# Kernel optimization log

Hardware: AMD Instinct MI355X
Metric: run time of the kernel (lower is better)

Reference implementation:

```python
import jax, jax.numpy as jnp
import numpy as np

NEIGH = 0.4  # neighborhood_size from the module


def setup_inputs() -> dict:
    key = jax.random.key(0)
    ks = jax.random.split(key, 14)
    N, E, H, G, M = 1024, 64, 128, 8, 20
    OUT = 6 * M
    f32 = jnp.float32
    inp = {
        "xabs": jax.random.uniform(ks[0], (N, 2), f32),
        "i_h0": jax.random.normal(ks[1], (1, N, H), f32) * 0.1,
        "i_c0": jax.random.normal(ks[2], (1, N, H), f32) * 0.1,
        # I_Embedding: Linear(2, E)
        "W_emb": jax.random.normal(ks[3], (E, 2), f32) * 0.5,
        "b_emb": jax.random.normal(ks[4], (E,), f32) * 0.1,
        # embedding_social: Linear(G*G*H, E)
        "W_soc": jax.random.normal(ks[5], (E, G * G * H), f32) * (1.0 / np.sqrt(G * G * H)),
        "b_soc": jax.random.normal(ks[6], (E,), f32) * 0.1,
        # LSTM(2E -> H), torch gate order [i, f, g, o]
        "W_ih": jax.random.normal(ks[7], (4 * H, 2 * E), f32) * (1.0 / np.sqrt(2 * E)),
        "W_hh": jax.random.normal(ks[8], (4 * H, H), f32) * (1.0 / np.sqrt(H)),
        "b_ih": jax.random.normal(ks[9], (4 * H,), f32) * 0.05,
        "b_hh": jax.random.normal(ks[10], (4 * H,), f32) * 0.05,
        # I_Output: Linear(H, 6*M)
        "W_out": jax.random.normal(ks[11], (OUT, H), f32) * (1.0 / np.sqrt(H)),
        "b_out": jax.random.normal(ks[12], (OUT,), f32) * 0.05,
    }
    return inp


def _grid_mask(xabs, G):
    # Vectorized getGridMask: [N, N, G*G] one-hot bin membership.
    N = xabs.shape[0]
    # dx[n, m] = other_x - width_low(n); in-range iff 0 <= dx < NEIGH
    dx = xabs[None, :, 0] - (xabs[:, None, 0] - NEIGH / 2)
    dy = xabs[None, :, 1] - (xabs[:, None, 1] - NEIGH / 2)
    cell_x = jnp.floor(dx / NEIGH * G).astype(jnp.int32)
    cell_y = jnp.floor(dy / NEIGH * G).astype(jnp.int32)
    valid = (dx >= 0) & (dx < NEIGH) & (dy >= 0) & (dy < NEIGH)
    valid &= (cell_x >= 0) & (cell_x < G) & (cell_y >= 0) & (cell_y < G)
    valid &= ~jnp.eye(N, dtype=bool)  # skip self
    cell = jnp.where(valid, cell_x + cell_y * G, 0)
    mask = jax.nn.one_hot(cell, G * G, dtype=xabs.dtype)
    return mask * valid[:, :, None].astype(xabs.dtype)


def reference(xabs, i_h0, i_c0, W_emb, b_emb, W_soc, b_soc,
              W_ih, W_hh, b_ih, b_hh, W_out, b_out):
    N = xabs.shape[0]
    H = i_h0.shape[-1]
    G = int(np.sqrt(W_soc.shape[1] // H))
    M = W_out.shape[0] // 6

    # Input embedding
    emb_x = jax.nn.relu(xabs @ W_emb.T + b_emb)  # [N, E]

    # Social pooling: grid mask + scatter-reduce of hidden states
    h0 = i_h0[0]  # [N, H]
    mask = _grid_mask(xabs, G)  # [N, N, G*G]
    social = jnp.einsum('nmg,md->ngd', mask, h0)  # [N, G*G, H]
    social = social.reshape(N, G * G * H)
    pooling = jax.nn.relu(social @ W_soc.T + b_soc)  # [N, E]

    # Single LSTM step (seq len 1, 1 layer), torch gate order i,f,g,o
    lstm_in = jnp.concatenate([emb_x, pooling], axis=-1)  # [N, 2E]
    gates = lstm_in @ W_ih.T + b_ih + h0 @ W_hh.T + b_hh  # [N, 4H]
    i_g, f_g, g_g, o_g = jnp.split(gates, 4, axis=-1)
    c = jax.nn.sigmoid(f_g) * i_c0[0] + jax.nn.sigmoid(i_g) * jnp.tanh(g_g)
    h = jax.nn.sigmoid(o_g) * jnp.tanh(c)  # [N, H]

    final = h @ W_out.T + b_out  # [N, 6M]
    mu1, mu2, log_sigma1, log_sigma2, rho, pi_logits = jnp.split(final, 6, axis=1)
    return (mu1, mu2, log_sigma1, log_sigma2, rho, pi_logits)
```

## Files before the change

kernel.cpp:

```cpp
#include <hip/hip_runtime.h>
#include <hip/hip_bf16.h>
#include <math.h>

typedef __hip_bfloat16 bf16;
typedef short s8v __attribute__((ext_vector_type(8)));
typedef float f4v __attribute__((ext_vector_type(4)));

__device__ __forceinline__ float b2f(bf16 v) { return __bfloat162float(v); }

template <bool F32>
__device__ __forceinline__ float ld(const void* p, int i) {
  if (F32) return ((const float*)p)[i];
  return b2f(((const bf16*)p)[i]);
}

template <bool F32>
__device__ __forceinline__ s8v ldfrag(const void* p, size_t i) {
  if (F32) {
    const float* f = (const float*)p + i;
    float4 u = *reinterpret_cast<const float4*>(f);
    float4 v = *reinterpret_cast<const float4*>(f + 4);
    s8v r;
    bf16 t;
    t = __float2bfloat16(u.x); r[0] = *(short*)&t;
    t = __float2bfloat16(u.y); r[1] = *(short*)&t;
    t = __float2bfloat16(u.z); r[2] = *(short*)&t;
    t = __float2bfloat16(u.w); r[3] = *(short*)&t;
    t = __float2bfloat16(v.x); r[4] = *(short*)&t;
    t = __float2bfloat16(v.y); r[5] = *(short*)&t;
    t = __float2bfloat16(v.z); r[6] = *(short*)&t;
    t = __float2bfloat16(v.w); r[7] = *(short*)&t;
    return r;
  }
  return *reinterpret_cast<const s8v*>((const bf16*)p + i);
}

__device__ __forceinline__ float sigm(float x) {
  return 0.5f * (1.0f + tanhf(0.5f * x));
}

__device__ __forceinline__ bool detect_f32(const void* xabs) {
  unsigned short v = ((const unsigned short*)xabs)[threadIdx.x & 63];
  int ex = (v >> 7) & 0xFF;
  return __ballot(ex >= 0x93) != 0ull;
}

template <bool F32>
__device__ __forceinline__ void cvt4(const void* src, bf16* __restrict__ dst,
                                     int count, int gt, int gsz) {
  for (int i = gt * 4; i < count; i += gsz * 4) {
    if (F32) {
      float4 v = *reinterpret_cast<const float4*>((const float*)src + i);
      bf16 t[4] = {__float2bfloat16(v.x), __float2bfloat16(v.y),
                   __float2bfloat16(v.z), __float2bfloat16(v.w)};
      *reinterpret_cast<uint2*>(&dst[i]) = *reinterpret_cast<uint2*>(t);
    } else {
      *reinterpret_cast<uint2*>(&dst[i]) =
          *reinterpret_cast<const uint2*>((const bf16*)src + i);
    }
  }
}

__global__ __launch_bounds__(256) void k_prep(const void* Wsoc, const void* Wih,
                                              const void* Whh, const void* Wout,
                                              bf16* Wsoc_b, bf16* Wih_b,
                                              bf16* Whh_b, bf16* Wout_b,
                                              const void* xabs) {
  const int gt = blockIdx.x * 256 + threadIdx.x;
  const int gsz = gridDim.x * 256;
  if (detect_f32(xabs)) {
    cvt4<true>(Wsoc, Wsoc_b, 64 * 8192, gt, gsz);
    cvt4<true>(Wih, Wih_b, 512 * 128, gt, gsz);
    cvt4<true>(Whh, Whh_b, 512 * 128, gt, gsz);
    cvt4<true>(Wout, Wout_b, 120 * 128, gt, gsz);
  } else {
    cvt4<false>(Wsoc, Wsoc_b, 64 * 8192, gt, gsz);
    cvt4<false>(Wih, Wih_b, 512 * 128, gt, gsz);
    cvt4<false>(Whh, Whh_b, 512 * 128, gt, gsz);
    cvt4<false>(Wout, Wout_b, 120 * 128, gt, gsz);
  }
}

template <bool F32>
__device__ __forceinline__ void zgemm_body(const void* h0,
                                           const bf16* __restrict__ Wsoc_b,
                                           bf16* __restrict__ Z) {
  const int wave = threadIdx.x >> 6, lane = threadIdx.x & 63;
  const int mt = blockIdx.x & 63;
  const int g  = (blockIdx.x >> 6) * 4 + wave;
  const int r16 = lane & 15, quad = lane >> 4;
  s8v afr[4];
#pragma unroll
  for (int kq = 0; kq < 4; ++kq)
    afr[kq] = ldfrag<F32>(h0, (size_t)(mt * 16 + r16) * 128 + kq * 32 + quad * 8);
  f4v acc[4] = {{0.f, 0.f, 0.f, 0.f}, {0.f, 0.f, 0.f, 0.f},
                {0.f, 0.f, 0.f, 0.f}, {0.f, 0.f, 0.f, 0.f}};
#pragma unroll
  for (int t = 0; t < 4; ++t) {
#pragma unroll
    for (int kq = 0; kq < 4; ++kq) {
      s8v bfr = *reinterpret_cast<const s8v*>(
          &Wsoc_b[(size_t)(t * 16 + r16) * 8192 + g * 128 + kq * 32 + quad * 8]);
      acc[t] = __builtin_amdgcn_mfma_f32_16x16x32_bf16(afr[kq], bfr, acc[t],
                                                       0, 0, 0);
    }
  }
#pragma unroll
  for (int t = 0; t < 4; ++t)
#pragma unroll
    for (int reg = 0; reg < 4; ++reg)
      Z[(size_t)(mt * 16 + quad * 4 + reg) * 4096 + g * 64 + t * 16 + r16] =
          __float2bfloat16(acc[t][reg]);
}

__global__ __launch_bounds__(256) void k_zgemm(const void* h0,
                                               const bf16* Wsoc_b,
                                               bf16* __restrict__ Z,
                                               const void* xabs) {
  if (detect_f32(xabs)) zgemm_body<true>(h0, Wsoc_b, Z);
  else                  zgemm_body<false>(h0, Wsoc_b, Z);
}

#define XS 264
#define HS 136

template <bool F32>
__device__ __forceinline__ void fused_body(
    const void* xabs, const void* h0, const void* Wemb, const void* bemb,
    const void* bsoc, const bf16* __restrict__ Wih_b,
    const bf16* __restrict__ Whh_b, const void* bih, const void* bhh,
    const void* c0, const bf16* __restrict__ Wout_b, const void* bout,
    const bf16* __restrict__ Z, void* out, char* smem) {
  float* G   = (float*)smem;
  int* lists = (int*)smem;
  bf16* Xb   = (bf16*)(smem + 32768);
  bf16* Hb   = (bf16*)(smem + 32768 + 16 * XS * 2);
  const int tid = threadIdx.x;
  const int wave = tid >> 6, lane = tid & 63;
  const int r16 = lane & 15, quad = lane >> 4;

  for (int idx = 4 * XS + tid; idx < 16 * XS; idx += 256)
    Xb[idx] = __float2bfloat16(0.f);
  for (int idx = 4 * HS + tid; idx < 16 * HS; idx += 256)
    Hb[idx] = __float2bfloat16(0.f);

  const int n = blockIdx.x * 4 + wave;
  const float xn = ld<F32>(xabs, 2 * n);
  const float yn = ld<F32>(xabs, 2 * n + 1);
  const float tx = xn - 0.2f, ty = yn - 0.2f;
  int* mylist = lists + wave * 1024;
  int cnt = 0;
  for (int c = 0; c < 16; ++c) {
    const int m = c * 64 + lane;
    float dx = ld<F32>(xabs, 2 * m) - tx;
    float dy = ld<F32>(xabs, 2 * m + 1) - ty;
    int cx = (int)floorf(dx / 0.4f * 8.0f);
    int cy = (int)floorf(dy / 0.4f * 8.0f);
    bool valid = (dx >= 0.f) & (dx < 0.4f) & (dy >= 0.f) & (dy < 0.4f) &
                 (cx >= 0) & (cx < 8) & (cy >= 0) & (cy < 8) & (m != n);
    unsigned long long msk = __ballot(valid);
    if (valid) {
      int pos = cnt + __popcll(msk & ((1ull << lane) - 1ull));
      mylist[pos] = (m << 6) | (cx + cy * 8);
    }
    cnt += __popcll(msk);
  }
  float a0 = 0.f, a1 = 0.f, a2 = 0.f, a3 = 0.f;
  float a4 = 0.f, a5 = 0.f, a6 = 0.f, a7 = 0.f;
  int i = 0;
  for (; i + 8 <= cnt; i += 8) {
    int e0 = mylist[i],     e1 = mylist[i + 1];
    int e2 = mylist[i + 2], e3 = mylist[i + 3];
    int e4 = mylist[i + 4], e5 = mylist[i + 5];
    int e6 = mylist[i + 6], e7 = mylist[i + 7];
    a0 += b2f(Z[(size_t)(e0 >> 6) * 4096 + (e0 & 63) * 64 + lane]);
    a1 += b2f(Z[(size_t)(e1 >> 6) * 4096 + (e1 & 63) * 64 + lane]);
    a2 += b2f(Z[(size_t)(e2 >> 6) * 4096 + (e2 & 63) * 64 + lane]);
    a3 += b2f(Z[(size_t)(e3 >> 6) * 4096 + (e3 & 63) * 64 + lane]);
    a4 += b2f(Z[(size_t)(e4 >> 6) * 4096 + (e4 & 63) * 64 + lane]);
    a5 += b2f(Z[(size_t)(e5 >> 6) * 4096 + (e5 & 63) * 64 + lane]);
    a6 += b2f(Z[(size_t)(e6 >> 6) * 4096 + (e6 & 63) * 64 + lane]);
    a7 += b2f(Z[(size_t)(e7 >> 6) * 4096 + (e7 & 63) * 64 + lane]);
  }
  for (; i < cnt; ++i) {
    int e0 = mylist[i];
    a0 += b2f(Z[(size_t)(e0 >> 6) * 4096 + (e0 & 63) * 64 + lane]);
  }
  float pool = ((a0 + a1) + (a2 + a3)) + ((a4 + a5) + (a6 + a7));
  pool = fmaxf(pool + ld<F32>(bsoc, lane), 0.f);
  float emb = fmaxf(ld<F32>(Wemb, lane * 2) * xn +
                        ld<F32>(Wemb, lane * 2 + 1) * yn + ld<F32>(bemb, lane),
                    0.f);
  Xb[wave * XS + lane] = __float2bfloat16(emb);
  Xb[wave * XS + 64 + lane] = __float2bfloat16(pool);
  Xb[wave * XS + 128 + lane] = __float2bfloat16(ld<F32>(h0, n * 128 + lane));
  Xb[wave * XS + 192 + lane] =
      __float2bfloat16(ld<F32>(h0, n * 128 + 64 + lane));
  __syncthreads();

  s8v afr[8];
#pragma unroll
  for (int kq = 0; kq < 8; ++kq)
    afr[kq] = *reinterpret_cast<const s8v*>(&Xb[r16 * XS + kq * 32 + quad * 8]);
  const int j0w = wave * 128;
  f4v bacc[8];
#pragma unroll
  for (int jt = 0; jt < 8; ++jt) bacc[jt] = (f4v){0.f, 0.f, 0.f, 0.f};
#pragma unroll
  for (int jt = 0; jt < 8; ++jt) {
    int j = j0w + jt * 16 + r16;
#pragma unroll
    for (int kq = 0; kq < 4; ++kq) {
      s8v bfr = *reinterpret_cast<const s8v*>(
          &Wih_b[(size_t)j * 128 + kq * 32 + quad * 8]);
      bacc[jt] = __builtin_amdgcn_mfma_f32_16x16x32_bf16(afr[kq], bfr, bacc[jt],
                                                         0, 0, 0);
    }
#pragma unroll
    for (int kq = 0; kq < 4; ++kq) {
      s8v bfr = *reinterpret_cast<const s8v*>(
          &Whh_b[(size_t)j * 128 + kq * 32 + quad * 8]);
      bacc[jt] = __builtin_amdgcn_mfma_f32_16x16x32_bf16(afr[kq + 4], bfr,
                                                         bacc[jt], 0, 0, 0);
    }
  }
#pragma unroll
  for (int jt = 0; jt < 8; ++jt) {
    int j = j0w + jt * 16 + r16;
    float bias = ld<F32>(bih, j) + ld<F32>(bhh, j);
#pragma unroll
    for (int reg = 0; reg < 4; ++reg)
      G[(quad * 4 + reg) * 512 + j] = bacc[jt][reg] + bias;
  }
  __syncthreads();

  for (int idx = tid; idx < 512; idx += 256) {
    int m = idx >> 7, tt = idx & 127;
    float ig = G[m * 512 + tt], fg = G[m * 512 + 128 + tt];
    float gg = G[m * 512 + 256 + tt], og = G[m * 512 + 384 + tt];
    float c = sigm(fg) * ld<F32>(c0, (blockIdx.x * 4 + m) * 128 + tt) +
              sigm(ig) * tanhf(gg);
    Hb[m * HS + tt] = __float2bfloat16(sigm(og) * tanhf(c));
  }
  __syncthreads();

  s8v hfr[4];
#pragma unroll
  for (int kq = 0; kq < 4; ++kq)
    hfr[kq] = *reinterpret_cast<const s8v*>(&Hb[r16 * HS + kq * 32 + quad * 8]);
#pragma unroll
  for (int jt2 = 0; jt2 < 2; ++jt2) {
    int j = wave * 32 + jt2 * 16 + r16;
    int jj = j < 120 ? j : 119;
    f4v oacc = (f4v){0.f, 0.f, 0.f, 0.f};
#pragma unroll
    for (int kq = 0; kq < 4; ++kq) {
      s8v bfr = *reinterpret_cast<const s8v*>(
          &Wout_b[(size_t)jj * 128 + kq * 32 + quad * 8]);
      oacc = __builtin_amdgcn_mfma_f32_16x16x32_bf16(hfr[kq], bfr, oacc, 0, 0, 0);
    }
    if (j < 120 && quad == 0) {
      float bo = ld<F32>(bout, j);
      int kk = j / 20, mm = j % 20;
#pragma unroll
      for (int reg = 0; reg < 4; ++reg) {
        int oi = kk * 20480 + (blockIdx.x * 4 + reg) * 20 + mm;
        float val = oacc[reg] + bo;
        if (F32) ((float*)out)[oi] = val;
        else     ((bf16*)out)[oi] = __float2bfloat16(val);
      }
    }
  }
}

__global__ __launch_bounds__(256, 1) void k_fused(
    const void* xabs, const void* h0, const void* Wemb, const void* bemb,
    const void* bsoc, const bf16* Wih_b, const bf16* Whh_b, const void* bih,
    const void* bhh, const void* c0, const bf16* Wout_b, const void* bout,
    const bf16* __restrict__ Z, void* out) {
  __shared__ __align__(16) char smem[32768 + 16 * XS * 2 + 16 * HS * 2];
  if (detect_f32(xabs))
    fused_body<true>(xabs, h0, Wemb, bemb, bsoc, Wih_b, Whh_b, bih, bhh, c0,
                     Wout_b, bout, Z, out, smem);
  else
    fused_body<false>(xabs, h0, Wemb, bemb, bsoc, Wih_b, Whh_b, bih, bhh, c0,
                      Wout_b, bout, Z, out, smem);
}

extern "C" void kernel_launch(void* const* d_in, const int* in_sizes, int n_in,
                              void* d_out, int out_size, void* d_ws, size_t ws_size,
                              hipStream_t stream) {
  const void* xabs = d_in[0];
  const void* h0   = d_in[1];
  const void* c0   = d_in[2];
  const void* Wemb = d_in[3];
  const void* bemb = d_in[4];
  const void* Wsoc = d_in[5];
  const void* bsoc = d_in[6];
  const void* Wih  = d_in[7];
  const void* Whh  = d_in[8];
  const void* bih  = d_in[9];
  const void* bhh  = d_in[10];
  const void* Wout = d_in[11];
  const void* bout = d_in[12];

  bf16* Z      = (bf16*)d_ws;
  bf16* Wsoc_b = Z + (size_t)1024 * 4096;
  bf16* Wih_b  = Wsoc_b + (size_t)64 * 8192;
  bf16* Whh_b  = Wih_b + (size_t)512 * 128;
  bf16* Wout_b = Whh_b + (size_t)512 * 128;

  k_prep<<<dim3(128), dim3(256), 0, stream>>>(Wsoc, Wih, Whh, Wout, Wsoc_b,
                                              Wih_b, Whh_b, Wout_b, xabs);
  k_zgemm<<<dim3(1024), dim3(256), 0, stream>>>(h0, Wsoc_b, Z, xabs);
  k_fused<<<dim3(256), dim3(256), 0, stream>>>(xabs, h0, Wemb, bemb, bsoc,
                                               Wih_b, Whh_b, bih, bhh, c0,
                                               Wout_b, bout, Z, d_out);
}
```

Before: 129.3 us.

## Fold weight conversion into Z-GEMM and raise per-block M tiling

```diff
diff --git a/kernel.cpp b/kernel.cpp
--- a/kernel.cpp
+++ b/kernel.cpp
@@ -61,64 +61,69 @@
   }
 }
 
-__global__ __launch_bounds__(256) void k_prep(const void* Wsoc, const void* Wih,
-                                              const void* Whh, const void* Wout,
-                                              bf16* Wsoc_b, bf16* Wih_b,
-                                              bf16* Whh_b, bf16* Wout_b,
-                                              const void* xabs) {
-  const int gt = blockIdx.x * 256 + threadIdx.x;
-  const int gsz = gridDim.x * 256;
-  if (detect_f32(xabs)) {
-    cvt4<true>(Wsoc, Wsoc_b, 64 * 8192, gt, gsz);
-    cvt4<true>(Wih, Wih_b, 512 * 128, gt, gsz);
-    cvt4<true>(Whh, Whh_b, 512 * 128, gt, gsz);
-    cvt4<true>(Wout, Wout_b, 120 * 128, gt, gsz);
-  } else {
-    cvt4<false>(Wsoc, Wsoc_b, 64 * 8192, gt, gsz);
-    cvt4<false>(Wih, Wih_b, 512 * 128, gt, gsz);
-    cvt4<false>(Whh, Whh_b, 512 * 128, gt, gsz);
-    cvt4<false>(Wout, Wout_b, 120 * 128, gt, gsz);
-  }
-}
-
-template <bool F32>
-__device__ __forceinline__ void zgemm_body(const void* h0,
-                                           const bf16* __restrict__ Wsoc_b,
-                                           bf16* __restrict__ Z) {
+template <bool F32>
+__device__ __forceinline__ void zgemm_body(const void* h0, const void* Wsoc,
+                                           const void* Wih, const void* Whh,
+                                           const void* Wout,
+                                           bf16* __restrict__ Z, bf16* Wih_b,
+                                           bf16* Whh_b, bf16* Wout_b) {
+  if (blockIdx.x >= 256) {
+    const int gt = (blockIdx.x - 256) * 256 + threadIdx.x;
+    const int gsz = 16 * 256;
+    cvt4<F32>(Wih, Wih_b, 512 * 128, gt, gsz);
+    cvt4<F32>(Whh, Whh_b, 512 * 128, gt, gsz);
+    cvt4<F32>(Wout, Wout_b, 120 * 128, gt, gsz);
+    return;
+  }
   const int wave = threadIdx.x >> 6, lane = threadIdx.x & 63;
-  const int mt = blockIdx.x & 63;
-  const int g  = (blockIdx.x >> 6) * 4 + wave;
+  const int mt = blockIdx.x & 15;
+  const int g  = (blockIdx.x >> 4) * 4 + wave;
   const int r16 = lane & 15, quad = lane >> 4;
-  s8v afr[4];
-#pragma unroll
-  for (int kq = 0; kq < 4; ++kq)
-    afr[kq] = ldfrag<F32>(h0, (size_t)(mt * 16 + r16) * 128 + kq * 32 + quad * 8);
-  f4v acc[4] = {{0.f, 0.f, 0.f, 0.f}, {0.f, 0.f, 0.f, 0.f},
-                {0.f, 0.f, 0.f, 0.f}, {0.f, 0.f, 0.f, 0.f}};
+
+  s8v afr[4][4];
+#pragma unroll
+  for (int ms = 0; ms < 4; ++ms)
+#pragma unroll
+    for (int kq = 0; kq < 4; ++kq)
+      afr[ms][kq] = ldfrag<F32>(
+          h0, (size_t)(mt * 64 + ms * 16 + r16) * 128 + kq * 32 + quad * 8);
+
+  f4v acc[4][4];
+#pragma unroll
+  for (int ms = 0; ms < 4; ++ms)
+#pragma unroll
+    for (int t = 0; t < 4; ++t) acc[ms][t] = (f4v){0.f, 0.f, 0.f, 0.f};
+
 #pragma unroll
   for (int t = 0; t < 4; ++t) {
 #pragma unroll
     for (int kq = 0; kq < 4; ++kq) {
-      s8v bfr = *reinterpret_cast<const s8v*>(
-          &Wsoc_b[(size_t)(t * 16 + r16) * 8192 + g * 128 + kq * 32 + quad * 8]);
-      acc[t] = __builtin_amdgcn_mfma_f32_16x16x32_bf16(afr[kq], bfr, acc[t],
-                                                       0, 0, 0);
-    }
-  }
-#pragma unroll
-  for (int t = 0; t < 4; ++t)
-#pragma unroll
-    for (int reg = 0; reg < 4; ++reg)
-      Z[(size_t)(mt * 16 + quad * 4 + reg) * 4096 + g * 64 + t * 16 + r16] =
-          __float2bfloat16(acc[t][reg]);
-}
-
-__global__ __launch_bounds__(256) void k_zgemm(const void* h0,
-                                               const bf16* Wsoc_b,
-                                               bf16* __restrict__ Z,
-                                               const void* xabs) {
-  if (detect_f32(xabs)) zgemm_body<true>(h0, Wsoc_b, Z);
-  else                  zgemm_body<false>(h0, Wsoc_b, Z);
+      s8v bfr = ldfrag<F32>(
+          Wsoc, (size_t)(t * 16 + r16) * 8192 + g * 128 + kq * 32 + quad * 8);
+#pragma unroll
+      for (int ms = 0; ms < 4; ++ms)
+        acc[ms][t] = __builtin_amdgcn_mfma_f32_16x16x32_bf16(afr[ms][kq], bfr,
+                                                             acc[ms][t], 0, 0, 0);
+    }
+  }
+#pragma unroll
+  for (int ms = 0; ms < 4; ++ms)
+#pragma unroll
+    for (int t = 0; t < 4; ++t)
+#pragma unroll
+      for (int reg = 0; reg < 4; ++reg)
+        Z[(size_t)(mt * 64 + ms * 16 + quad * 4 + reg) * 4096 + g * 64 +
+          t * 16 + r16] = __float2bfloat16(acc[ms][t][reg]);
+}
+
+__global__ __launch_bounds__(256, 1) void k_zgemm(
+    const void* h0, const void* Wsoc, const void* Wih, const void* Whh,
+    const void* Wout, bf16* __restrict__ Z, bf16* Wih_b, bf16* Whh_b,
+    bf16* Wout_b, const void* xabs) {
+  if (detect_f32(xabs))
+    zgemm_body<true>(h0, Wsoc, Wih, Whh, Wout, Z, Wih_b, Whh_b, Wout_b);
+  else
+    zgemm_body<false>(h0, Wsoc, Wih, Whh, Wout, Z, Wih_b, Whh_b, Wout_b);
 }
 
 #define XS 264
@@ -305,14 +310,12 @@
   const void* bout = d_in[12];
 
   bf16* Z      = (bf16*)d_ws;
-  bf16* Wsoc_b = Z + (size_t)1024 * 4096;
-  bf16* Wih_b  = Wsoc_b + (size_t)64 * 8192;
+  bf16* Wih_b  = Z + (size_t)1024 * 4096;
   bf16* Whh_b  = Wih_b + (size_t)512 * 128;
   bf16* Wout_b = Whh_b + (size_t)512 * 128;
 
-  k_prep<<<dim3(128), dim3(256), 0, stream>>>(Wsoc, Wih, Whh, Wout, Wsoc_b,
-                                              Wih_b, Whh_b, Wout_b, xabs);
-  k_zgemm<<<dim3(1024), dim3(256), 0, stream>>>(h0, Wsoc_b, Z, xabs);
+  k_zgemm<<<dim3(272), dim3(256), 0, stream>>>(h0, Wsoc, Wih, Whh, Wout, Z,
+                                               Wih_b, Whh_b, Wout_b, xabs);
   k_fused<<<dim3(256), dim3(256), 0, stream>>>(xabs, h0, Wemb, bemb, bsoc,
                                                Wih_b, Whh_b, bih, bhh, c0,
                                                Wout_b, bout, Z, d_out);
```

New measurement: 124.3 us, median of 2. -3.9%, faster.
